# Optimization experiments

Measured on AMD Instinct MI355X. Metric: run time of the kernel, lower is better.

## Reference

```python
import jax, jax.numpy as jnp
import numpy as np

DIM = 512
HEADS = 8
HD = DIM // HEADS

def _rotate_half(t):
    t1, t2 = jnp.split(t, 2, axis=-1)
    return jnp.concatenate((-t2, t1), axis=-1)

def _layernorm(x, g, b, eps=1e-5):
    mu = jnp.mean(x, axis=-1, keepdims=True)
    var = jnp.var(x, axis=-1, keepdims=True)
    return (x - mu) * jax.lax.rsqrt(var + eps) * g + b

def setup_inputs() -> dict:
    key = jax.random.key(0)
    ks = jax.random.split(key, 12)
    B, S = 4, 2048
    x = jax.random.normal(ks[0], (B, S, DIM), dtype=jnp.float32)
    rope_cos = jax.random.uniform(ks[1], (1, S, 1, HD), dtype=jnp.float32)
    rope_sin = jax.random.uniform(ks[2], (1, S, 1, HD), dtype=jnp.float32)
    sd = 1.0 / np.sqrt(DIM)
    params = {
        'norm1_g': jnp.ones((DIM,), jnp.float32),
        'norm1_b': jnp.zeros((DIM,), jnp.float32),
        'norm2_g': jnp.ones((DIM,), jnp.float32),
        'norm2_b': jnp.zeros((DIM,), jnp.float32),
        'w_qkv': jax.random.uniform(ks[3], (DIM, 3 * DIM), jnp.float32, -sd, sd),
        'b_qkv': jax.random.uniform(ks[4], (3 * DIM,), jnp.float32, -sd, sd),
        'w_proj': jax.random.uniform(ks[5], (DIM, DIM), jnp.float32, -sd, sd),
        'b_proj': jax.random.uniform(ks[6], (DIM,), jnp.float32, -sd, sd),
        'w_fc1': jax.random.uniform(ks[7], (DIM, 4 * DIM), jnp.float32, -sd, sd),
        'b_fc1': jax.random.uniform(ks[8], (4 * DIM,), jnp.float32, -sd, sd),
        'w_fc2': jax.random.uniform(ks[9], (4 * DIM, DIM), jnp.float32, -1.0 / np.sqrt(4 * DIM), 1.0 / np.sqrt(4 * DIM)),
        'b_fc2': jax.random.uniform(ks[10], (DIM,), jnp.float32, -1.0 / np.sqrt(4 * DIM), 1.0 / np.sqrt(4 * DIM)),
    }
    return {'x': x, 'rope_cos': rope_cos, 'rope_sin': rope_sin, **params}

def reference(x, rope_cos, rope_sin, norm1_g, norm1_b, norm2_g, norm2_b,
              w_qkv, b_qkv, w_proj, b_proj, w_fc1, b_fc1, w_fc2, b_fc2):
    B, S, D = x.shape
    scale = 1.0 / np.sqrt(HD)
    shortcut = x
    h = _layernorm(x, norm1_g, norm1_b)
    qkv = (h @ w_qkv + b_qkv).reshape(B, S, 3, HEADS, HD)
    q, k, v = qkv[:, :, 0], qkv[:, :, 1], qkv[:, :, 2]  # [B,S,H,hd]
    q = q * rope_cos + _rotate_half(q) * rope_sin
    k = k * rope_cos + _rotate_half(k) * rope_sin
    # attention over heads: scores [B,H,S,S]
    attn = jnp.einsum('bqhd,bkhd->bhqk', q, k) * scale
    attn = jax.nn.softmax(attn, axis=-1)
    o = jnp.einsum('bhqk,bkhd->bqhd', attn, v).reshape(B, S, D)
    o = o @ w_proj + b_proj
    x = shortcut + o  # dropout is identity in eval
    h2 = _layernorm(x, norm2_g, norm2_b)
    mlp = jax.nn.gelu(h2 @ w_fc1 + b_fc1, approximate=False) @ w_fc2 + b_fc2
    return x + mlp
```

## Files before the change

kernel.cpp:

```cpp
#include <hip/hip_runtime.h>
#include <cstdint>
#include <cstddef>

typedef unsigned short u16;
typedef unsigned int   u32;
typedef __bf16 bf16x8 __attribute__((ext_vector_type(8)));
typedef float  f32x4  __attribute__((ext_vector_type(4)));

#define BS   8192
#define DIMM 512
#define NH   8
#define HD   64
#define SEQ  2048
#define DFF  2048
#define NQKV 1536

#define GLD16(g, l) __builtin_amdgcn_global_load_lds( \
    (__attribute__((address_space(1))) const void*)(g), \
    (__attribute__((address_space(3))) void*)(l), 16, 0, 0)

#define SBAR   __builtin_amdgcn_s_barrier()
#define VMCNT4 asm volatile("s_waitcnt vmcnt(4)" ::: "memory")
#define VMCNT0 asm volatile("s_waitcnt vmcnt(0)" ::: "memory")
#define LGKM0  asm volatile("s_waitcnt lgkmcnt(0)" ::: "memory")

__device__ __forceinline__ float b2f(u16 s) {
  u32 u = ((u32)s) << 16;
  float f; __builtin_memcpy(&f, &u, 4); return f;
}
__device__ __forceinline__ u16 f2b(float f) {
  u32 u; __builtin_memcpy(&u, &f, 4);
  u += 0x7fffu + ((u >> 16) & 1u);
  return (u16)(u >> 16);
}
__device__ __forceinline__ u16 f2b_rtz(float f) {
  u32 u; __builtin_memcpy(&u, &f, 4);
  return (u16)(u >> 16);
}

#define SZ_QKV (DIMM * NQKV)
#define SZ_PRJ (DIMM * DIMM)
#define SZ_F1  (DIMM * DFF)
#define SZ_F2  (DFF * DIMM)
__global__ __launch_bounds__(256) void transpose_all_k(
    const float* __restrict__ w_qkv, const float* __restrict__ w_prj,
    const float* __restrict__ w_f1,  const float* __restrict__ w_f2,
    u16* __restrict__ o_qkv, u16* __restrict__ o_prj,
    u16* __restrict__ o_f1,  u16* __restrict__ o_f2) {
  int idx = blockIdx.x * 256 + threadIdx.x;
  const float* W; u16* O; int Kd, Nd, off;
  if (idx < SZ_QKV)                         { W = w_qkv; O = o_qkv; Kd = DIMM; Nd = NQKV; off = idx; }
  else if (idx < SZ_QKV + SZ_PRJ)           { W = w_prj; O = o_prj; Kd = DIMM; Nd = DIMM; off = idx - SZ_QKV; }
  else if (idx < SZ_QKV + SZ_PRJ + SZ_F1)   { W = w_f1;  O = o_f1;  Kd = DIMM; Nd = DFF;  off = idx - SZ_QKV - SZ_PRJ; }
  else                                      { W = w_f2;  O = o_f2;  Kd = DFF;  Nd = DIMM; off = idx - SZ_QKV - SZ_PRJ - SZ_F1; }
  int n = off / Kd, k = off - n * Kd;
  O[off] = f2b(W[(size_t)k * Nd + n]);
}

__global__ __launch_bounds__(256) void ln_f32b_k(const float* __restrict__ X,
    const float* __restrict__ G, const float* __restrict__ Bb, u16* __restrict__ out) {
  int w = threadIdx.x >> 6, lane = threadIdx.x & 63;
  size_t row = (size_t)blockIdx.x * 4 + w;
  const float* xr = X + row * DIMM;
  float v[8];
  *(float4*)&v[0] = *(const float4*)(xr + lane * 8);
  *(float4*)&v[4] = *(const float4*)(xr + lane * 8 + 4);
  float s = 0.f, s2 = 0.f;
#pragma unroll
  for (int j = 0; j < 8; j++) { s += v[j]; s2 += v[j] * v[j]; }
#pragma unroll
  for (int m = 1; m < 64; m <<= 1) { s += __shfl_xor(s, m); s2 += __shfl_xor(s2, m); }
  float mu = s * (1.f / DIMM);
  float rsd = rsqrtf(s2 * (1.f / DIMM) - mu * mu + 1e-5f);
  float g[8], bb[8];
  *(float4*)&g[0]  = *(const float4*)(G + lane * 8);
  *(float4*)&g[4]  = *(const float4*)(G + lane * 8 + 4);
  *(float4*)&bb[0] = *(const float4*)(Bb + lane * 8);
  *(float4*)&bb[4] = *(const float4*)(Bb + lane * 8 + 4);
  uint4 ov; u16* os = (u16*)&ov;
#pragma unroll
  for (int j = 0; j < 8; j++) os[j] = f2b((v[j] - mu) * rsd * g[j] + bb[j]);
  *(uint4*)(out + row * DIMM + lane * 8) = ov;
}

template <int EPI, int TM, int TN, int BK>
__global__ __launch_bounds__(256) void gemm_bt(const u16* __restrict__ A,
    const u16* __restrict__ BT, const float* __restrict__ bias,
    void* __restrict__ Cout, const float* __restrict__ resid, int N, int Kd) {
  constexpr int CPR  = BK / 8;
  constexpr int CPRB = (BK == 64) ? 3 : 2;
  constexpr int RS   = (BK == 64) ? 0 : 1;
  constexpr int KK   = BK / 32;
  constexpr int WROWS = (TN == 128) ? TM / 2 : TM / 4;
  constexpr int MT   = WROWS / 16;
  constexpr int ALOOP = TM * CPR / 256;
  constexpr int BLOOP = TN * CPR / 256;
  __shared__ __align__(16) u16 a_s[2][TM * BK];
  __shared__ __align__(16) u16 b_s[2][TN * BK];
  int t = threadIdx.x, lane = t & 63, w = t >> 6;
  int l15 = lane & 15, quad = lane >> 4;
  int gx = gridDim.x;
  int lid = blockIdx.x + gx * blockIdx.y;
  int per = (gx * gridDim.y) >> 3;
  int nid = (lid & 7) * per + (lid >> 3);
  int bx = nid % gx, by = nid / gx;
  int m0 = by * TM, n0 = bx * TN;
  int wm = (TN == 128) ? (w >> 1) * WROWS : w * WROWS;
  int wn = (TN == 128) ? (w & 1) * 64 : 0;
  f32x4 z4 = {0.f, 0.f, 0.f, 0.f};
  f32x4 acc[MT][4];
#pragma unroll
  for (int i = 0; i < MT; i++)
#pragma unroll
    for (int j = 0; j < 4; j++) acc[i][j] = z4;

#define GSTAGE(buf, ts) do {                                                  \
    int k0_ = (ts) * BK;                                                      \
    _Pragma("unroll")                                                         \
    for (int i = 0; i < ALOOP; i++) {                                         \
      int c_ = t + i * 256;                                                   \
      int row_ = c_ >> CPRB, pos_ = c_ & (CPR - 1);                           \
      int ch_ = (pos_ ^ (row_ >> RS)) & (CPR - 1);                            \
      GLD16(A + (size_t)(m0 + row_) * Kd + k0_ + ch_ * 8, &a_s[buf][c_ * 8]); \
    }                                                                         \
    _Pragma("unroll")                                                         \
    for (int i = 0; i < BLOOP; i++) {                                         \
      int c_ = t + i * 256;                                                   \
      int row_ = c_ >> CPRB, pos_ = c_ & (CPR - 1);                           \
      int ch_ = (pos_ ^ (row_ >> RS)) & (CPR - 1);                            \
      GLD16(BT + (size_t)(n0 + row_) * Kd + k0_ + ch_ * 8, &b_s[buf][c_ * 8]);\
    }                                                                         \
  } while (0)

#define GFRAG(buf) do {                                                       \
    _Pragma("unroll")                                                         \
    for (int mt = 0; mt < MT; mt++) {                                         \
      _Pragma("unroll")                                                       \
      for (int kk = 0; kk < KK; kk++) {                                       \
        int row_ = wm + mt * 16 + l15;                                        \
        int pos_ = ((kk * 4 + quad) ^ (row_ >> RS)) & (CPR - 1);              \
        af[mt][kk] = *(const bf16x8*)&a_s[buf][row_ * BK + pos_ * 8];         \
      }                                                                       \
    }                                                                         \
    _Pragma("unroll")                                                         \
    for (int nt = 0; nt < 4; nt++) {                                          \
      _Pragma("unroll")                                                       \
      for (int kk = 0; kk < KK; kk++) {                                       \
        int row_ = wn + nt * 16 + l15;                                        \
        int pos_ = ((kk * 4 + quad) ^ (row_ >> RS)) & (CPR - 1);              \
        bfm[nt][kk] = *(const bf16x8*)&b_s[buf][row_ * BK + pos_ * 8];        \
      }                                                                       \
    }                                                                         \
  } while (0)

#define GMFMA() do {                                                          \
    _Pragma("unroll")                                                         \
    for (int kk = 0; kk < KK; kk++)                                           \
      _Pragma("unroll")                                                       \
      for (int mt = 0; mt < MT; mt++)                                         \
        _Pragma("unroll")                                                     \
        for (int nt = 0; nt < 4; nt++)                                        \
          acc[mt][nt] = __builtin_amdgcn_mfma_f32_16x16x32_bf16(              \
              af[mt][kk], bfm[nt][kk], acc[mt][nt], 0, 0, 0);                 \
  } while (0)

  bf16x8 af[MT][KK], bfm[4][KK];
  GSTAGE(0, 0);
  GSTAGE(1, 1);
  VMCNT4;
  SBAR;
  int nsteps = Kd / BK;
  for (int ts = 0; ts < nsteps; ts += 2) {
    GFRAG(0);
    LGKM0;
    SBAR;
    if (ts + 2 < nsteps) {
      GSTAGE(0, ts + 2);
      GMFMA();
      VMCNT4;
    } else {
      GMFMA();
      VMCNT0;
    }
    SBAR;
    GFRAG(1);
    LGKM0;
    SBAR;
    if (ts + 3 < nsteps) {
      GSTAGE(1, ts + 3);
      GMFMA();
      VMCNT4;
    } else {
      GMFMA();
      VMCNT0;
    }
    SBAR;
  }
#undef GSTAGE
#undef GFRAG
#undef GMFMA

#pragma unroll
  for (int nt = 0; nt < 4; nt++) {
    int col = n0 + wn + nt * 16 + l15;
    float bv = bias[col];
#pragma unroll
    for (int mt = 0; mt < MT; mt++) {
#pragma unroll
      for (int r = 0; r < 4; r++) {
        int rw = m0 + wm + mt * 16 + quad * 4 + r;
        float v = acc[mt][nt][r] + bv;
        size_t off = (size_t)rw * N + col;
        if (EPI == 0) {
          ((float*)Cout)[off] = v;
        } else if (EPI == 1) {
          ((float*)Cout)[off] = v + resid[off];
        } else if (EPI == 2) {
          ((u16*)Cout)[off] = f2b(0.5f * v * (1.f + erff(v * 0.70710678118654752f)));
        } else {
          ((u16*)Cout)[off] = f2b(v);
        }
      }
    }
  }
}

#define QSCALE 0.18033688f
__global__ __launch_bounds__(256) void rope_k(const u16* __restrict__ qkv,
    const float* __restrict__ C, const float* __restrict__ Sn,
    u16* __restrict__ Qo, u16* __restrict__ Ko, u16* __restrict__ Vo) {
  int idx = blockIdx.x * 256 + threadIdx.x;
  int row = idx / 192;
  int cn = idx - row * 192;
  int n0 = cn * 8;
  int comp = n0 >> 9;
  int hh = (n0 >> 6) & 7;
  int d0 = n0 & 63;
  int b = row >> 11, s = row & 2047;
  const u16* src = qkv + (size_t)row * NQKV;
  uint4 val = *(const uint4*)(src + n0);
  u16* vs = (u16*)&val;
  size_t oo = ((size_t)((b << 3) + hh) * SEQ + s) * HD + d0;
  if (comp == 2) { *(uint4*)(Vo + oo) = val; return; }
  uint4 pv = *(const uint4*)(src + (n0 ^ 32));
  u16* ps = (u16*)&pv;
  float cv[8], sv[8];
  *(float4*)&cv[0] = *(const float4*)(C + s * HD + d0);
  *(float4*)&cv[4] = *(const float4*)(C + s * HD + d0 + 4);
  *(float4*)&sv[0] = *(const float4*)(Sn + s * HD + d0);
  *(float4*)&sv[4] = *(const float4*)(Sn + s * HD + d0 + 4);
  float sgn = (d0 & 32) ? 1.f : -1.f;
  float sc = (comp == 0) ? QSCALE : 1.f;
  uint4 ov; u16* os = (u16*)&ov;
#pragma unroll
  for (int j = 0; j < 8; j++)
    os[j] = f2b(sc * (b2f(vs[j]) * cv[j] + sgn * b2f(ps[j]) * sv[j]));
  *(uint4*)((comp == 0 ? Qo : Ko) + oo) = ov;
}

__global__ __launch_bounds__(256) void vtrans_k(const u16* __restrict__ V,
                                                u16* __restrict__ Vt) {
  __shared__ u16 ld[64 * 72];
  int t = threadIdx.x;
  int bh = blockIdx.x >> 5;
  int s0 = (blockIdx.x & 31) * 64;
  const u16* src = V + (size_t)bh * SEQ * HD + (size_t)s0 * HD;
  u16* dst = Vt + (size_t)bh * SEQ * HD;
#pragma unroll
  for (int i = 0; i < 2; i++) {
    int c = t + i * 256, s = c >> 3, cp = c & 7;
    *(uint4*)&ld[s * 72 + ((cp ^ (s >> 3)) << 3)] =
        *(const uint4*)(src + (size_t)s * HD + cp * 8);
  }
  __syncthreads();
#pragma unroll
  for (int i = 0; i < 2; i++) {
    int c = t + i * 256, d = c >> 3, sc = c & 7;
    uint4 ov; u16* os = (u16*)&ov;
#pragma unroll
    for (int j = 0; j < 8; j++) {
      int s = sc * 8 + j;
      os[j] = ld[s * 72 + (((d >> 3) ^ (s >> 3)) << 3) + (d & 7)];
    }
    *(uint4*)(dst + (size_t)d * SEQ + s0 + sc * 8) = ov;
  }
}

__global__ __launch_bounds__(512) void attn_flash_k(const u16* __restrict__ Qg,
    const u16* __restrict__ Kg, const u16* __restrict__ Vtg,
    float* __restrict__ Op, float* __restrict__ Lp) {
  __shared__ u16 q_s[128 * 72];
  __shared__ u16 k_s[64 * 72];
  __shared__ u16 vt_s[64 * 72];
  int t = threadIdx.x, lane = t & 63, w = t >> 6;
  int l15 = lane & 15, quad = lane >> 4;
  int lid = blockIdx.x;
  int nid = (lid & 7) * 128 + (lid >> 3);
  int bhh = nid >> 4;
  int bh = bhh >> 1, half = bhh & 1;
  int qt0 = (nid & 15) * 128;
  int kt0 = half << 10;
  int b = bh >> 3, h = bh & 7;
  const u16* Qp = Qg + (size_t)bh * SEQ * HD;
  const u16* Kp = Kg + (size_t)bh * SEQ * HD;
  const u16* Vp = Vtg + (size_t)bh * SEQ * HD;
  int row = t >> 3, ch = t & 7;

  int sW = (w * 4 + quad) & 7;
  int pcol[4];
#pragma unroll
  for (int n = 0; n < 4; n++)
    pcol[n] = (((n * 2 + (l15 >> 3)) ^ sW) << 3) + (l15 & 7);
  int sR = (w * 4 + (l15 >> 2)) & 7;
  int pch[2];
#pragma unroll
  for (int kk = 0; kk < 2; kk++)
    pch[kk] = ((kk * 4 + quad) ^ sR) << 3;

#pragma unroll
  for (int i = 0; i < 2; i++) {
    int c = t + i * 512, qr = c >> 3, qc = c & 7;
    *(uint4*)&q_s[qr * 72 + qc * 8] = *(const uint4*)(Qp + (size_t)(qt0 + qr) * HD + qc * 8);
  }
  uint4 kr = *(const uint4*)(Kp + (size_t)(kt0 + row) * HD + ch * 8);
  uint4 vr = *(const uint4*)(Vp + (size_t)row * SEQ + kt0 + ch * 8);
  __syncthreads();
  bf16x8 qa[2];
  qa[0] = *(const bf16x8*)&q_s[(w * 16 + l15) * 72 + quad * 8];
  qa[1] = *(const bf16x8*)&q_s[(w * 16 + l15) * 72 + 32 + quad * 8];
  u16* p_s = q_s;
  f32x4 z4 = {0.f, 0.f, 0.f, 0.f};
  f32x4 of[4];
#pragma unroll
  for (int n = 0; n < 4; n++) of[n] = z4;
  float lrun[4] = {};

  for (int kt = kt0; kt < kt0 + 1024; kt += 64) {
    __syncthreads();
    *(uint4*)&k_s[row * 72 + ch * 8] = kr;
    *(uint4*)&vt_s[row * 72 + ch * 8] = vr;
    __syncthreads();
    if (kt + 64 < kt0 + 1024) {
      kr = *(const uint4*)(Kp + (size_t)(kt + 64 + row) * HD + ch * 8);
      vr = *(const uint4*)(Vp + (size_t)row * SEQ + kt + 64 + ch * 8);
    }
    f32x4 sf[4];
#pragma unroll
    for (int n = 0; n < 4; n++) sf[n] = z4;
    __builtin_amdgcn_s_setprio(1);
#pragma unroll
    for (int kk = 0; kk < 2; kk++)
#pragma unroll
      for (int n = 0; n < 4; n++) {
        bf16x8 kb = *(const bf16x8*)&k_s[(n * 16 + l15) * 72 + kk * 32 + quad * 8];
        sf[n] = __builtin_amdgcn_mfma_f32_16x16x32_bf16(qa[kk], kb, sf[n], 0, 0, 0);
      }
    __builtin_amdgcn_s_setprio(0);
#pragma unroll
    for (int r = 0; r < 4; r++) {
      int prow = (w * 16 + quad * 4 + r) * 72;
#pragma unroll
      for (int n = 0; n < 4; n++) {
        float pp = exp2f(sf[n][r]);
        lrun[r] += pp;
        p_s[prow + pcol[n]] = f2b_rtz(pp);
      }
    }
    __builtin_amdgcn_s_setprio(1);
#pragma unroll
    for (int kk = 0; kk < 2; kk++) {
      bf16x8 pa = *(const bf16x8*)&p_s[(w * 16 + l15) * 72 + pch[kk]];
#pragma unroll
      for (int n = 0; n < 4; n++) {
        bf16x8 vb = *(const bf16x8*)&vt_s[(n * 16 + l15) * 72 + kk * 32 + quad * 8];
        of[n] = __builtin_amdgcn_mfma_f32_16x16x32_bf16(pa, vb, of[n], 0, 0, 0);
      }
    }
    __builtin_amdgcn_s_setprio(0);
  }
  float* Opb = Op + (size_t)half * ((size_t)BS * DIMM);
  float* Lpb = Lp + (size_t)half * (32 * 2048);
#pragma unroll
  for (int r = 0; r < 4; r++) {
    float l = lrun[r];
#pragma unroll
    for (int m = 1; m < 16; m <<= 1) l += __shfl_xor(l, m);
    int s = qt0 + w * 16 + quad * 4 + r;
    size_t orow = (size_t)b * SEQ + s;
#pragma unroll
    for (int n = 0; n < 4; n++)
      Opb[orow * DIMM + h * HD + n * 16 + l15] = of[n][r];
    if (l15 == 0) Lpb[(bh << 11) + s] = l;
  }
}

__global__ __launch_bounds__(256) void attn_combine_k(const float* __restrict__ Op,
    const float* __restrict__ Lp, u16* __restrict__ ob) {
  int idx = blockIdx.x * 256 + threadIdx.x;
  size_t off8 = (size_t)idx * 8;
  int row = (int)(off8 >> 9), col = (int)(off8 & 511);
  int h = col >> 6;
  int b = row >> 11, s = row & 2047;
  int li = (((b << 3) + h) << 11) + s;
  float inv = 1.f / (Lp[li] + Lp[li + (32 << 11)]);
  const float* O0 = Op + off8;
  const float* O1 = Op + (size_t)BS * DIMM + off8;
  float4 a0 = *(const float4*)(O0);
  float4 a1 = *(const float4*)(O0 + 4);
  float4 c0 = *(const float4*)(O1);
  float4 c1 = *(const float4*)(O1 + 4);
  uint4 ov; u16* os = (u16*)&ov;
  os[0] = f2b((a0.x + c0.x) * inv); os[1] = f2b((a0.y + c0.y) * inv);
  os[2] = f2b((a0.z + c0.z) * inv); os[3] = f2b((a0.w + c0.w) * inv);
  os[4] = f2b((a1.x + c1.x) * inv); os[5] = f2b((a1.y + c1.y) * inv);
  os[6] = f2b((a1.z + c1.z) * inv); os[7] = f2b((a1.w + c1.w) * inv);
  *(uint4*)(ob + off8) = ov;
}

extern "C" void kernel_launch(void* const* d_in, const int* in_sizes, int n_in,
                              void* d_out, int out_size, void* d_ws, size_t ws_size,
                              hipStream_t stream) {
  const float* x    = (const float*)d_in[0];
  const float* rc   = (const float*)d_in[1];
  const float* rsn  = (const float*)d_in[2];
  const float* n1g  = (const float*)d_in[3];
  const float* n1b  = (const float*)d_in[4];
  const float* n2g  = (const float*)d_in[5];
  const float* n2b  = (const float*)d_in[6];
  const float* wqkv = (const float*)d_in[7];
  const float* bqkv = (const float*)d_in[8];
  const float* wprj = (const float*)d_in[9];
  const float* bprj = (const float*)d_in[10];
  const float* wf1  = (const float*)d_in[11];
  const float* bf1  = (const float*)d_in[12];
  const float* wf2  = (const float*)d_in[13];
  const float* bf2  = (const float*)d_in[14];

  char* p = (char*)d_ws;
  u16*   wqkvT = (u16*)p;
  u16*   wprjT = (u16*)(p + (2u  << 20));
  u16*   wf1T  = (u16*)(p + (3u  << 20));
  u16*   wf2T  = (u16*)(p + (5u  << 20));
  u16*   h1    = (u16*)(p + (8u  << 20));
  u16*   qkvb  = (u16*)(p + (16u << 20));
  float* Opart = (float*)(p + (16u << 20));
  u16*   Vt    = (u16*)(p + (48u << 20));
  float* Lpart = (float*)(p + (56u << 20));
  u16*   Qb    = (u16*)(p + (64u << 20));
  u16*   Kb    = (u16*)(p + (72u << 20));
  u16*   Vb    = (u16*)(p + (80u << 20));
  float* x2    = (float*)(p + (88u << 20));
  u16*   ob    = h1;
  u16*   h2    = h1;
  u16*   mid   = qkvb;

  transpose_all_k<<<dim3((SZ_QKV + SZ_PRJ + SZ_F1 + SZ_F2) / 256), 256, 0, stream>>>(
      wqkv, wprj, wf1, wf2, wqkvT, wprjT, wf1T, wf2T);

  ln_f32b_k<<<dim3(BS / 4), 256, 0, stream>>>(x, n1g, n1b, h1);

  gemm_bt<3, 128, 128, 32><<<dim3(NQKV / 128, BS / 128), 256, 0, stream>>>(h1, wqkvT, bqkv, qkvb, nullptr, NQKV, DIMM);

  rope_k<<<dim3(BS * NQKV / 8 / 256), 256, 0, stream>>>(qkvb, rc, rsn, Qb, Kb, Vb);

  vtrans_k<<<dim3(32 * (SEQ / 64)), 256, 0, stream>>>(Vb, Vt);

  attn_flash_k<<<dim3(2 * 32 * (SEQ / 128)), 512, 0, stream>>>(Qb, Kb, Vt, Opart, Lpart);

  attn_combine_k<<<dim3(BS * DIMM / 8 / 256), 256, 0, stream>>>(Opart, Lpart, ob);

  gemm_bt<1, 64, 64, 64><<<dim3(DIMM / 64, BS / 64), 256, 0, stream>>>(ob, wprjT, bprj, x2, x, DIMM, DIMM);

  ln_f32b_k<<<dim3(BS / 4), 256, 0, stream>>>(x2, n2g, n2b, h2);

  gemm_bt<2, 128, 128, 32><<<dim3(DFF / 128, BS / 128), 256, 0, stream>>>(h2, wf1T, bf1, mid, nullptr, DFF, DIMM);

  gemm_bt<1, 64, 64, 64><<<dim3(DIMM / 64, BS / 64), 256, 0, stream>>>(mid, wf2T, bf2, (float*)d_out, x2, DIMM, DFF);
}
```

Baseline: 345.9 us.

## Double query rows per wave in flash attention to reuse K/V tiles

Each wave now handles 32 query rows (two 16-row subtiles) instead of 16, so the block covers 256 queries and the grid halves. Every K and V fragment read from LDS feeds two MFMAs, which cuts LDS traffic and global K/V reloads per query. In exchange each thread holds more accumulators and registers, and the grid drops to 512 blocks of 512 threads, which may lower occupancy and load balance across CUs.

```diff
diff --git a/kernel.cpp b/kernel.cpp
--- a/kernel.cpp
+++ b/kernel.cpp
@@ -289,16 +289,16 @@
 __global__ __launch_bounds__(512) void attn_flash_k(const u16* __restrict__ Qg,
     const u16* __restrict__ Kg, const u16* __restrict__ Vtg,
     float* __restrict__ Op, float* __restrict__ Lp) {
-  __shared__ u16 q_s[128 * 72];
+  __shared__ u16 q_s[256 * 72];
   __shared__ u16 k_s[64 * 72];
   __shared__ u16 vt_s[64 * 72];
   int t = threadIdx.x, lane = t & 63, w = t >> 6;
   int l15 = lane & 15, quad = lane >> 4;
   int lid = blockIdx.x;
-  int nid = (lid & 7) * 128 + (lid >> 3);
-  int bhh = nid >> 4;
+  int nid = (lid & 7) * 64 + (lid >> 3);
+  int bhh = nid >> 3;
   int bh = bhh >> 1, half = bhh & 1;
-  int qt0 = (nid & 15) * 128;
+  int qt0 = (nid & 7) * 256;
   int kt0 = half << 10;
   int b = bh >> 3, h = bh & 7;
   const u16* Qp = Qg + (size_t)bh * SEQ * HD;
@@ -306,34 +306,41 @@
   const u16* Vp = Vtg + (size_t)bh * SEQ * HD;
   int row = t >> 3, ch = t & 7;
 
-  int sW = (w * 4 + quad) & 7;
-  int pcol[4];
-#pragma unroll
-  for (int n = 0; n < 4; n++)
-    pcol[n] = (((n * 2 + (l15 >> 3)) ^ sW) << 3) + (l15 & 7);
-  int sR = (w * 4 + (l15 >> 2)) & 7;
-  int pch[2];
-#pragma unroll
-  for (int kk = 0; kk < 2; kk++)
-    pch[kk] = ((kk * 4 + quad) ^ sR) << 3;
-
-#pragma unroll
-  for (int i = 0; i < 2; i++) {
+  int pcol[2][4], pch[2][2];
+#pragma unroll
+  for (int rs = 0; rs < 2; rs++) {
+    int sW = (rs * 4 + quad) & 7;
+    int sR = (rs * 4 + (l15 >> 2)) & 7;
+#pragma unroll
+    for (int n = 0; n < 4; n++)
+      pcol[rs][n] = (((n * 2 + (l15 >> 3)) ^ sW) << 3) + (l15 & 7);
+#pragma unroll
+    for (int kk = 0; kk < 2; kk++)
+      pch[rs][kk] = ((kk * 4 + quad) ^ sR) << 3;
+  }
+
+#pragma unroll
+  for (int i = 0; i < 4; i++) {
     int c = t + i * 512, qr = c >> 3, qc = c & 7;
     *(uint4*)&q_s[qr * 72 + qc * 8] = *(const uint4*)(Qp + (size_t)(qt0 + qr) * HD + qc * 8);
   }
   uint4 kr = *(const uint4*)(Kp + (size_t)(kt0 + row) * HD + ch * 8);
   uint4 vr = *(const uint4*)(Vp + (size_t)row * SEQ + kt0 + ch * 8);
   __syncthreads();
-  bf16x8 qa[2];
-  qa[0] = *(const bf16x8*)&q_s[(w * 16 + l15) * 72 + quad * 8];
-  qa[1] = *(const bf16x8*)&q_s[(w * 16 + l15) * 72 + 32 + quad * 8];
+  bf16x8 qa[2][2];
+#pragma unroll
+  for (int rs = 0; rs < 2; rs++) {
+    qa[rs][0] = *(const bf16x8*)&q_s[(w * 32 + rs * 16 + l15) * 72 + quad * 8];
+    qa[rs][1] = *(const bf16x8*)&q_s[(w * 32 + rs * 16 + l15) * 72 + 32 + quad * 8];
+  }
   u16* p_s = q_s;
   f32x4 z4 = {0.f, 0.f, 0.f, 0.f};
-  f32x4 of[4];
-#pragma unroll
-  for (int n = 0; n < 4; n++) of[n] = z4;
-  float lrun[4] = {};
+  f32x4 of[2][4];
+#pragma unroll
+  for (int rs = 0; rs < 2; rs++)
+#pragma unroll
+    for (int n = 0; n < 4; n++) of[rs][n] = z4;
+  float lrun[2][4] = {};
 
   for (int kt = kt0; kt < kt0 + 1024; kt += 64) {
     __syncthreads();
@@ -344,36 +351,43 @@
       kr = *(const uint4*)(Kp + (size_t)(kt + 64 + row) * HD + ch * 8);
       vr = *(const uint4*)(Vp + (size_t)row * SEQ + kt + 64 + ch * 8);
     }
-    f32x4 sf[4];
-#pragma unroll
-    for (int n = 0; n < 4; n++) sf[n] = z4;
+    f32x4 sf[2][4];
+#pragma unroll
+    for (int rs = 0; rs < 2; rs++)
+#pragma unroll
+      for (int n = 0; n < 4; n++) sf[rs][n] = z4;
     __builtin_amdgcn_s_setprio(1);
 #pragma unroll
     for (int kk = 0; kk < 2; kk++)
 #pragma unroll
       for (int n = 0; n < 4; n++) {
         bf16x8 kb = *(const bf16x8*)&k_s[(n * 16 + l15) * 72 + kk * 32 + quad * 8];
-        sf[n] = __builtin_amdgcn_mfma_f32_16x16x32_bf16(qa[kk], kb, sf[n], 0, 0, 0);
+        sf[0][n] = __builtin_amdgcn_mfma_f32_16x16x32_bf16(qa[0][kk], kb, sf[0][n], 0, 0, 0);
+        sf[1][n] = __builtin_amdgcn_mfma_f32_16x16x32_bf16(qa[1][kk], kb, sf[1][n], 0, 0, 0);
       }
     __builtin_amdgcn_s_setprio(0);
 #pragma unroll
-    for (int r = 0; r < 4; r++) {
-      int prow = (w * 16 + quad * 4 + r) * 72;
-#pragma unroll
-      for (int n = 0; n < 4; n++) {
-        float pp = exp2f(sf[n][r]);
-        lrun[r] += pp;
-        p_s[prow + pcol[n]] = f2b_rtz(pp);
+    for (int rs = 0; rs < 2; rs++)
+#pragma unroll
+      for (int r = 0; r < 4; r++) {
+        int prow = (w * 32 + rs * 16 + quad * 4 + r) * 72;
+#pragma unroll
+        for (int n = 0; n < 4; n++) {
+          float pp = exp2f(sf[rs][n][r]);
+          lrun[rs][r] += pp;
+          p_s[prow + pcol[rs][n]] = f2b_rtz(pp);
+        }
       }
-    }
     __builtin_amdgcn_s_setprio(1);
 #pragma unroll
     for (int kk = 0; kk < 2; kk++) {
-      bf16x8 pa = *(const bf16x8*)&p_s[(w * 16 + l15) * 72 + pch[kk]];
+      bf16x8 pa0 = *(const bf16x8*)&p_s[(w * 32 + l15) * 72 + pch[0][kk]];
+      bf16x8 pa1 = *(const bf16x8*)&p_s[(w * 32 + 16 + l15) * 72 + pch[1][kk]];
 #pragma unroll
       for (int n = 0; n < 4; n++) {
         bf16x8 vb = *(const bf16x8*)&vt_s[(n * 16 + l15) * 72 + kk * 32 + quad * 8];
-        of[n] = __builtin_amdgcn_mfma_f32_16x16x32_bf16(pa, vb, of[n], 0, 0, 0);
+        of[0][n] = __builtin_amdgcn_mfma_f32_16x16x32_bf16(pa0, vb, of[0][n], 0, 0, 0);
+        of[1][n] = __builtin_amdgcn_mfma_f32_16x16x32_bf16(pa1, vb, of[1][n], 0, 0, 0);
       }
     }
     __builtin_amdgcn_s_setprio(0);
@@ -381,17 +395,19 @@
   float* Opb = Op + (size_t)half * ((size_t)BS * DIMM);
   float* Lpb = Lp + (size_t)half * (32 * 2048);
 #pragma unroll
-  for (int r = 0; r < 4; r++) {
-    float l = lrun[r];
-#pragma unroll
-    for (int m = 1; m < 16; m <<= 1) l += __shfl_xor(l, m);
-    int s = qt0 + w * 16 + quad * 4 + r;
-    size_t orow = (size_t)b * SEQ + s;
-#pragma unroll
-    for (int n = 0; n < 4; n++)
-      Opb[orow * DIMM + h * HD + n * 16 + l15] = of[n][r];
-    if (l15 == 0) Lpb[(bh << 11) + s] = l;
-  }
+  for (int rs = 0; rs < 2; rs++)
+#pragma unroll
+    for (int r = 0; r < 4; r++) {
+      float l = lrun[rs][r];
+#pragma unroll
+      for (int m = 1; m < 16; m <<= 1) l += __shfl_xor(l, m);
+      int s = qt0 + w * 32 + rs * 16 + quad * 4 + r;
+      size_t orow = (size_t)b * SEQ + s;
+#pragma unroll
+      for (int n = 0; n < 4; n++)
+        Opb[orow * DIMM + h * HD + n * 16 + l15] = of[rs][n][r];
+      if (l15 == 0) Lpb[(bh << 11) + s] = l;
+    }
 }
 
 __global__ __launch_bounds__(256) void attn_combine_k(const float* __restrict__ Op,
@@ -465,7 +481,7 @@
 
   vtrans_k<<<dim3(32 * (SEQ / 64)), 256, 0, stream>>>(Vb, Vt);
 
-  attn_flash_k<<<dim3(2 * 32 * (SEQ / 128)), 512, 0, stream>>>(Qb, Kb, Vt, Opart, Lpart);
+  attn_flash_k<<<dim3(2 * 32 * (SEQ / 256)), 512, 0, stream>>>(Qb, Kb, Vt, Opart, Lpart);
 
   attn_combine_k<<<dim3(BS * DIMM / 8 / 256), 256, 0, stream>>>(Opart, Lpart, ob);
 
```

Result: no change. 348.7 us (+0.8%).
